# Kernel tuning notes

Hardware: AMD Instinct MI355X
Metric: run time of the kernel (lower is better)

Reference implementation:

```python
import jax, jax.numpy as jnp
import numpy as np

N_CAND = 21  # tf.linspace(0, 1, 21) candidate pool
SOFTMIN_TEMP = 100.0


def _tree_constants(max_depth: int):
    """Signed split->descendant matrix M (S,N) and node->parent one-hot P (N,N)."""
    n_splits = 2 ** max_depth - 1
    n_nodes = 2 ** (max_depth + 1) - 1
    M = np.zeros((n_splits, n_nodes), np.float32)
    for s in range(n_splits):
        for n in range(n_nodes):
            a = n
            while a > 0:
                p = (a - 1) // 2
                if p == s:
                    # left-subtree descendants get -1, right-subtree +1
                    M[s, n] = -1.0 if a == 2 * s + 1 else 1.0
                    break
                a = p
    P = np.zeros((n_nodes, n_nodes), np.float32)
    for i in range(1, n_nodes):
        P[i, (i - 1) // 2] = 1.0
    return jnp.asarray(M), jnp.asarray(P), n_splits, n_nodes


def setup_inputs() -> dict:
    key = jax.random.key(0)
    kx, kw, kb = jax.random.split(key, 3)
    B, F = 512, 512
    max_depth = 8
    n_splits = 2 ** max_depth - 1
    x = jax.random.normal(kx, (B, F), dtype=jnp.float32)
    # VarianceScaling(scale=2.0, mode='fan_in') ~ std sqrt(2/F)
    W = jax.random.normal(kw, (F, n_splits), dtype=jnp.float32) * np.sqrt(2.0 / F).astype(np.float32)
    # keras RandomNormal default stddev=0.05
    b = jax.random.normal(kb, (n_splits,), dtype=jnp.float32) * 0.05
    return {"x": x, "W": W, "b": b, "max_depth": max_depth}


def reference(x, W, b, max_depth):
    M, P, n_splits, n_nodes = _tree_constants(int(max_depth))
    # q per split, then min over ancestor splits (method 0)
    q_split = x @ W + b                                   # (B, S)
    q_bsn = q_split[:, :, None] * M[None] + 1.0 - jnp.abs(M)[None]  # (B, S, N)
    q_node = jnp.min(q_bsn, axis=1)                       # (B, N)

    a_cand = jnp.linspace(0.0, 1.0, N_CAND)               # (C,)
    qn = q_node[:, :, None]                               # (B, N, 1)
    sqr = jnp.where(a_cand <= qn + 0.5, (a_cand - (qn + 0.5)) ** 2, 0.0)
    # reg part sums over the size-1 leading axis of a -> just a^2 (reg_lambda=1.0 in call)
    g_a = 0.5 * a_cand ** 2 + 0.5 * jnp.sum(sqr, axis=0)  # (N, C)

    eye = jnp.eye(n_nodes, dtype=jnp.float32)

    def body(carry, _):
        n2g, _ = carry
        g_grp = n2g.T @ g_a                               # (N, C): group-summed objective
        w = jax.nn.softmax(-SOFTMIN_TEMP * g_grp, axis=1)
        a_grp = jnp.sum(a_cand * w, axis=1)               # (N,) soft argmin over candidates
        a_node = n2g @ a_grp                              # (N,) broadcast group value to nodes
        a_par = (P @ a_node)[1:]
        a_par = jnp.concatenate([jnp.ones((1,), a_node.dtype), a_par])
        viol = a_node - a_par
        t = jnp.argmax(viol)
        cond = (jnp.max(viol) <= 1e-8) & (t > 0)
        t_oh = jax.nn.one_hot(t, n_nodes, dtype=jnp.float32)
        p_oh = t_oh @ P
        n2g = n2g + jnp.where(cond, 1.0, 0.0) * jnp.outer(t_oh, p_oh - t_oh)
        return (n2g, a_node), None

    (_, a_node), _ = jax.lax.scan(body, (eye, jnp.zeros(n_nodes, jnp.float32)), None,
                                  length=n_nodes + 1)
    trajectory = jnp.clip(q_node, 0.0, a_node[None, :])   # (B, N)
    return trajectory
```

## Files before the change

kernel.cpp:

```cpp
#include <hip/hip_runtime.h>
#include <hip/hip_bf16.h>
#include <math.h>

#define BATCH 512
#define FDIM  512
#define NSPL  255
#define NNOD  511
#define NC    21


__global__ __launch_bounds__(256) void k_qgemm(const float* __restrict__ x,
                                               const float* __restrict__ W,
                                               float* __restrict__ partial,
                                               int fpc) {
  __shared__ float Ws[64 * 68];
  __shared__ float xT[64 * 68];
  const int tid = threadIdx.x;
  const int s0 = blockIdx.x * 64;
  const int b0 = blockIdx.y * 64;
  const int f0 = blockIdx.z * fpc;
  const int sx = tid & 15;
  const int by = tid >> 4;
  float acc[4][4];
#pragma unroll
  for (int i = 0; i < 4; ++i)
#pragma unroll
    for (int j = 0; j < 4; ++j) acc[i][j] = 0.f;

  for (int fc = f0; fc < f0 + fpc; fc += 64) {
    {
      int si = tid & 63, fr = tid >> 6;
#pragma unroll
      for (int r = 0; r < 16; ++r) {
        int fi = fr + r * 4;
        int s = s0 + si;
        Ws[fi * 68 + si] = (s < NSPL) ? W[(fc + fi) * NSPL + s] : 0.f;
      }
      int j = tid & 63, ir = tid >> 6;
#pragma unroll
      for (int r = 0; r < 16; ++r) {
        int i = ir + r * 4;
        xT[j * 68 + i] = x[(b0 + i) * FDIM + (fc + j)];
      }
    }
    __syncthreads();
#pragma unroll 8
    for (int f = 0; f < 64; ++f) {
      float4 av = *(const float4*)&Ws[f * 68 + sx * 4];
      float4 xv = *(const float4*)&xT[f * 68 + by * 4];
      const float a4[4] = {av.x, av.y, av.z, av.w};
      const float x4[4] = {xv.x, xv.y, xv.z, xv.w};
#pragma unroll
      for (int i = 0; i < 4; ++i)
#pragma unroll
        for (int j = 0; j < 4; ++j) acc[i][j] += a4[i] * x4[j];
    }
    __syncthreads();
  }

  float* pout = partial + (size_t)blockIdx.z * (256 * BATCH);
#pragma unroll
  for (int i = 0; i < 4; ++i) {
    int s = s0 + sx * 4 + i;
    if (s < NSPL) {
      float4 v = make_float4(acc[i][0], acc[i][1], acc[i][2], acc[i][3]);
      *(float4*)&pout[s * BATCH + b0 + by * 4] = v;
    }
  }
}

__global__ __launch_bounds__(256) void k_qreduce(const float* __restrict__ partial,
                                                 const float* __restrict__ bias,
                                                 float* __restrict__ qsT, int n) {
  int idx = blockIdx.x * 256 + threadIdx.x;
  if (idx >= NSPL * BATCH) return;
  int s = idx >> 9;
  float v = 0.f;
  for (int c = 0; c < n; ++c) v += partial[(size_t)c * (256 * BATCH) + idx];
  qsT[idx] = v + bias[s];
}

__global__ __launch_bounds__(256) void k_qsplitT_fb(const float* __restrict__ x,
                                                    const float* __restrict__ W,
                                                    const float* __restrict__ bias,
                                                    float* __restrict__ qsT) {
  const int s = threadIdx.x;
  const int b0 = blockIdx.x * 8;
  if (s >= NSPL) return;
  float acc0[8], acc1[8];
#pragma unroll
  for (int i = 0; i < 8; ++i) { acc0[i] = 0.f; acc1[i] = 0.f; }
#pragma unroll 2
  for (int f = 0; f < 256; ++f) {
    float w0 = W[f * NSPL + s];
    float w1 = W[(f + 256) * NSPL + s];
#pragma unroll
    for (int i = 0; i < 8; ++i) {
      acc0[i] += x[(b0 + i) * FDIM + f] * w0;
      acc1[i] += x[(b0 + i) * FDIM + f + 256] * w1;
    }
  }
  float bs = bias[s];
#pragma unroll
  for (int i = 0; i < 8; ++i) qsT[s * BATCH + b0 + i] = (acc0[i] + acc1[i]) + bs;
}

__device__ __forceinline__ float qnode_walk(const float* __restrict__ qsT, int n, int b) {
  float q = 1.0f;
  int a = n;
  while (a > 0) {
    int p = (a - 1) >> 1;
    float v = qsT[p * BATCH + b];
    q = fminf(q, (a & 1) ? -v : v);
    a = p;
  }
  return q;
}

__global__ __launch_bounds__(256) void k_ga(const float* __restrict__ qsT,
                                            float* __restrict__ ga,
                                            double* __restrict__ agrp0,
                                            float* __restrict__ qnodeT) {
  const int n = blockIdx.x;
  const int tid = threadIdx.x;
  __shared__ float qs[BATCH];
  __shared__ double part[4][NC];
  __shared__ float gaRow[NC];
  __shared__ double zS[NC];
  __shared__ double eS[NC];
  __shared__ double mS;
#pragma unroll
  for (int rep = 0; rep < 2; ++rep) {
    int b = tid + rep * 256;
    float q = qnode_walk(qsT, n, b);
    qs[b] = q;
    qnodeT[n * BATCH + b] = q;
  }
  __syncthreads();
  if (tid < 4 * NC) {
    int c = tid % NC, chunk = tid / NC;
    double ac = 0.05 * (double)c;
    double ssum = 0.0;
    int b0 = chunk * 128;
    for (int b = b0; b < b0 + 128; ++b) {
      float qh = qs[b] + 0.5f;
      double dqh = (double)qh;
      if (ac <= dqh) { double d = ac - dqh; ssum += d * d; }
    }
    part[chunk][c] = ssum;
  }
  __syncthreads();
  if (tid < NC) {
    double ac = 0.05 * (double)tid;
    double ssum = ((part[0][tid] + part[1][tid]) + part[2][tid]) + part[3][tid];
    float gv = (float)(0.5 * ac * ac + 0.5 * ssum);
    ga[n * NC + tid] = gv;
    gaRow[tid] = gv;
  }
  __syncthreads();

  if (tid < NC) zS[tid] = -100.0 * (double)gaRow[tid];
  __syncthreads();
  if (tid == 0) {
    double m = -1e300;
#pragma unroll
    for (int c = 0; c < NC; ++c) m = fmax(m, zS[c]);
    mS = m;
  }
  __syncthreads();
  if (tid < NC) eS[tid] = exp(zS[tid] - mS);
  __syncthreads();
  if (tid == 0) {
    double S = 0.0;
#pragma unroll
    for (int c = 0; c < NC; ++c) S += eS[c];
    double A = 0.0;
#pragma unroll
    for (int c = 0; c < NC; ++c) A += (0.05 * (double)c) * (eS[c] / S);
    agrp0[n] = A;
  }
}

__global__ __launch_bounds__(64) void k_scan(const float* __restrict__ ga_g,
                                             const double* __restrict__ agrp0,
                                             double* __restrict__ a_node_out) {
  __shared__ float gaS[NNOD * NC];
  __shared__ double agrp[512];
  __shared__ double anode[512];
  __shared__ float kfS[512];
  const int lane = threadIdx.x;

  {
    const float4* src = (const float4*)ga_g;
    float4* dst = (float4*)gaS;
    const int n4 = (NNOD * NC) / 4;
#pragma unroll 4
    for (int i = lane; i < n4; i += 64) dst[i] = src[i];
    if (lane < (NNOD * NC) - n4 * 4) gaS[n4 * 4 + lane] = ga_g[n4 * 4 + lane];
  }
  for (int i = lane; i < 512; i += 64) {
    agrp[i] = (i < NNOD) ? agrp0[i] : 0.0;
    anode[i] = 0.0;
    kfS[i] = 0.0f;
  }
  __syncthreads();

  int t = 0, p = 0;
  double areg[8];
  int iter = 0;
  for (;;) {
    if (iter > 0) {
      int j = lane >> 5, c = lane & 31;
      int g = j ? p : t;
      double z = -1e300;
      if (c < NC) {
        double acc = (1.0 - (double)kfS[g]) * (double)gaS[g * NC + c];
        int l = 2 * g + 1, r = 2 * g + 2;
        if (l < NNOD) acc = acc + (double)kfS[l] * (double)gaS[l * NC + c];
        if (r < NNOD) acc = acc + (double)kfS[r] * (double)gaS[r * NC + c];
        z = -100.0 * acc;
      }
      double m = z;
#pragma unroll
      for (int off = 16; off >= 1; off >>= 1) m = fmax(m, __shfl_xor(m, off, 32));
      double e = (c < NC) ? exp(z - m) : 0.0;
      double S = e;
#pragma unroll
      for (int off = 16; off >= 1; off >>= 1) S += __shfl_xor(S, off, 32);
      double term = (c < NC) ? (0.05 * (double)c) * (e / S) : 0.0;
#pragma unroll
      for (int off = 16; off >= 1; off >>= 1) term += __shfl_xor(term, off, 32);
      if (c == 0) agrp[g] = term;
      __syncthreads();
    }

#pragma unroll
    for (int u = 0; u < 8; ++u) {
      int n = lane + (u << 6);
      if (n < NNOD) {
        double kn = (double)kfS[n];
        double agn = agrp[n];
        double an;
        if (n == 0) an = agn;
        else an = kn * agrp[(n - 1) >> 1] + (1.0 - kn) * agn;
        areg[u] = an;
        anode[n] = an;
      }
    }
    __syncthreads();

    double bv = -1e300; int bi = 0x7fffffff;
#pragma unroll
    for (int u = 0; u < 8; ++u) {
      int n = lane + (u << 6);
      if (n < NNOD) {
        double ap = (n == 0) ? 1.0 : anode[(n - 1) >> 1];
        double vi = areg[u] - ap;
        if (vi > bv) { bv = vi; bi = n; }
      }
    }
#pragma unroll
    for (int off = 32; off >= 1; off >>= 1) {
      double ov = __shfl_xor(bv, off, 64);
      int oi = __shfl_xor(bi, off, 64);
      if (ov > bv || (ov == bv && oi < bi)) { bv = ov; bi = oi; }
    }

    bool cond = (bv <= 1e-8) && (bi > 0);
    if (!cond || iter == 511) break;
    t = bi; p = (t - 1) >> 1;
    if (lane == 0) kfS[t] += 1.0f;
    __syncthreads();
    ++iter;
  }

#pragma unroll
  for (int u = 0; u < 8; ++u) {
    int n = lane + (u << 6);
    if (n < NNOD) a_node_out[n] = areg[u];
  }
}

__global__ __launch_bounds__(256) void k_clip(const float* __restrict__ qnodeT,
                                              const double* __restrict__ a_node,
                                              float* __restrict__ out) {
  __shared__ float tile[64][65];
  __shared__ double anS[64];
  const int n0 = blockIdx.x * 64;
  const int b0 = blockIdx.y * 64;
  const int tid = threadIdx.x;
  if (tid < 64) anS[tid] = (n0 + tid < NNOD) ? a_node[n0 + tid] : 0.0;
  for (int i = tid; i < 64 * 64; i += 256) {
    int ni = i >> 6, bj = i & 63;
    int nn = n0 + ni;
    tile[ni][bj] = (nn < NNOD) ? qnodeT[nn * BATCH + b0 + bj] : 0.f;
  }
  __syncthreads();
  for (int i = tid; i < 64 * 64; i += 256) {
    int bi = i >> 6, nj = i & 63;
    int nn = n0 + nj;
    if (nn < NNOD) {
      float q = tile[nj][bi];
      double r = fmin(fmax((double)q, 0.0), anS[nj]);
      out[(size_t)(b0 + bi) * NNOD + nn] = (float)r;
    }
  }
}

extern "C" void kernel_launch(void* const* d_in, const int* in_sizes, int n_in,
                              void* d_out, int out_size, void* d_ws, size_t ws_size,
                              hipStream_t stream) {
  (void)in_sizes; (void)n_in; (void)out_size;
  const float* x    = (const float*)d_in[0];
  const float* W    = (const float*)d_in[1];
  const float* bias = (const float*)d_in[2];
  float* out = (float*)d_out;

  char* ws = (char*)d_ws;
  const size_t PART_STRIDE = 256 * BATCH * sizeof(float);
  const size_t QS = 524288;
  const size_t QN = 1048576;
  const size_t GA = 43008;
  const size_t AG = 4096;
  const size_t AN = 4096;
  const size_t TAIL = QS + QN + GA + AG + AN;

  int n = 8;
  while (n > 1 && (size_t)n * PART_STRIDE + TAIL > ws_size) n >>= 1;
  bool splitk_ok = ((size_t)n * PART_STRIDE + TAIL <= ws_size);

  size_t P = splitk_ok ? (size_t)n * PART_STRIDE : 0;
  float*  qsT    = (float*) (ws + P);
  float*  qnodeT = (float*) (ws + P + QS);
  float*  ga     = (float*) (ws + P + QS + QN);
  double* agrp0  = (double*)(ws + P + QS + QN + GA);
  double* a_node = (double*)(ws + P + QS + QN + GA + AG);

  if (splitk_ok) {
    float* partial = (float*)ws;
    k_qgemm<<<dim3(4, 8, n), dim3(256), 0, stream>>>(x, W, partial, 512 / n);
    k_qreduce<<<dim3(510), dim3(256), 0, stream>>>(partial, bias, qsT, n);
  } else {
    k_qsplitT_fb<<<dim3(64), dim3(256), 0, stream>>>(x, W, bias, qsT);
  }
  k_ga<<<dim3(NNOD), dim3(256), 0, stream>>>(qsT, ga, agrp0, qnodeT);
  k_scan<<<dim3(1), dim3(64), 0, stream>>>(ga, agrp0, a_node);
  k_clip<<<dim3(8, 8), dim3(256), 0, stream>>>(qnodeT, a_node, out);
}
```

Measured before the change: 96.31 us.

## Replace split-K GEMM plus reduce with single-pass GEMM writing qsT directly

The split-K GEMM, which wrote partial sums to workspace, and its separate reduction kernel are replaced by one kernel. That kernel covers the full feature dimension per block, with a 16-split by 64-batch tile, and adds the bias before writing qsT. This removes one kernel launch and the round trip of the partial buffers through global memory. In exchange, each thread does far less register reuse (1x4 per thread instead of 4x4), so each output costs more shared-memory loads. The grid becomes 128 blocks with no split-K parallelism, and the GEMM runs serially over K.

```diff
diff --git a/kernel.cpp b/kernel.cpp
--- a/kernel.cpp
+++ b/kernel.cpp
@@ -9,32 +9,32 @@
 #define NC    21
 
 
-__global__ __launch_bounds__(256) void k_qgemm(const float* __restrict__ x,
-                                               const float* __restrict__ W,
-                                               float* __restrict__ partial,
-                                               int fpc) {
-  __shared__ float Ws[64 * 68];
+__global__ __launch_bounds__(256) void k_qgemm2(const float* __restrict__ x,
+                                                const float* __restrict__ W,
+                                                const float* __restrict__ bias,
+                                                float* __restrict__ qsT) {
+  __shared__ float Ws[64 * 17];
   __shared__ float xT[64 * 68];
   const int tid = threadIdx.x;
-  const int s0 = blockIdx.x * 64;
+  const int s0 = blockIdx.x * 16;
   const int b0 = blockIdx.y * 64;
-  const int f0 = blockIdx.z * fpc;
-  const int sx = tid & 15;
-  const int by = tid >> 4;
-  float acc[4][4];
-#pragma unroll
-  for (int i = 0; i < 4; ++i)
-#pragma unroll
-    for (int j = 0; j < 4; ++j) acc[i][j] = 0.f;
-
-  for (int fc = f0; fc < f0 + fpc; fc += 64) {
+  const int sl = tid >> 4;
+  const int bq = tid & 15;
+  const int s = s0 + sl;
+
+  float acc[4];
+  float vsum[4];
+#pragma unroll
+  for (int j = 0; j < 4; ++j) { acc[j] = 0.f; vsum[j] = 0.f; }
+
+  for (int fc = 0; fc < FDIM; fc += 64) {
     {
-      int si = tid & 63, fr = tid >> 6;
-#pragma unroll
-      for (int r = 0; r < 16; ++r) {
-        int fi = fr + r * 4;
-        int s = s0 + si;
-        Ws[fi * 68 + si] = (s < NSPL) ? W[(fc + fi) * NSPL + s] : 0.f;
+      int si = tid & 15, f4 = tid >> 4;
+#pragma unroll
+      for (int r = 0; r < 4; ++r) {
+        int fi = f4 + r * 16;
+        int ss = s0 + si;
+        Ws[fi * 17 + si] = (ss < NSPL) ? W[(fc + fi) * NSPL + ss] : 0.f;
       }
       int j = tid & 63, ir = tid >> 6;
 #pragma unroll
@@ -46,38 +46,23 @@
     __syncthreads();
 #pragma unroll 8
     for (int f = 0; f < 64; ++f) {
-      float4 av = *(const float4*)&Ws[f * 68 + sx * 4];
-      float4 xv = *(const float4*)&xT[f * 68 + by * 4];
-      const float a4[4] = {av.x, av.y, av.z, av.w};
+      float w = Ws[f * 17 + sl];
+      float4 xv = *(const float4*)&xT[f * 68 + bq * 4];
       const float x4[4] = {xv.x, xv.y, xv.z, xv.w};
 #pragma unroll
-      for (int i = 0; i < 4; ++i)
-#pragma unroll
-        for (int j = 0; j < 4; ++j) acc[i][j] += a4[i] * x4[j];
-    }
+      for (int j = 0; j < 4; ++j) acc[j] += w * x4[j];
+    }
+#pragma unroll
+    for (int j = 0; j < 4; ++j) { vsum[j] += acc[j]; acc[j] = 0.f; }
     __syncthreads();
   }
 
-  float* pout = partial + (size_t)blockIdx.z * (256 * BATCH);
-#pragma unroll
-  for (int i = 0; i < 4; ++i) {
-    int s = s0 + sx * 4 + i;
-    if (s < NSPL) {
-      float4 v = make_float4(acc[i][0], acc[i][1], acc[i][2], acc[i][3]);
-      *(float4*)&pout[s * BATCH + b0 + by * 4] = v;
-    }
-  }
-}
-
-__global__ __launch_bounds__(256) void k_qreduce(const float* __restrict__ partial,
-                                                 const float* __restrict__ bias,
-                                                 float* __restrict__ qsT, int n) {
-  int idx = blockIdx.x * 256 + threadIdx.x;
-  if (idx >= NSPL * BATCH) return;
-  int s = idx >> 9;
-  float v = 0.f;
-  for (int c = 0; c < n; ++c) v += partial[(size_t)c * (256 * BATCH) + idx];
-  qsT[idx] = v + bias[s];
+  if (s < NSPL) {
+    float bs = bias[s];
+#pragma unroll
+    for (int j = 0; j < 4; ++j)
+      qsT[s * BATCH + b0 + bq * 4 + j] = vsum[j] + bs;
+  }
 }
 
 __global__ __launch_bounds__(256) void k_qsplitT_fb(const float* __restrict__ x,
@@ -317,32 +302,18 @@
   float* out = (float*)d_out;
 
   char* ws = (char*)d_ws;
-  const size_t PART_STRIDE = 256 * BATCH * sizeof(float);
   const size_t QS = 524288;
   const size_t QN = 1048576;
   const size_t GA = 43008;
   const size_t AG = 4096;
-  const size_t AN = 4096;
-  const size_t TAIL = QS + QN + GA + AG + AN;
-
-  int n = 8;
-  while (n > 1 && (size_t)n * PART_STRIDE + TAIL > ws_size) n >>= 1;
-  bool splitk_ok = ((size_t)n * PART_STRIDE + TAIL <= ws_size);
-
-  size_t P = splitk_ok ? (size_t)n * PART_STRIDE : 0;
-  float*  qsT    = (float*) (ws + P);
-  float*  qnodeT = (float*) (ws + P + QS);
-  float*  ga     = (float*) (ws + P + QS + QN);
-  double* agrp0  = (double*)(ws + P + QS + QN + GA);
-  double* a_node = (double*)(ws + P + QS + QN + GA + AG);
-
-  if (splitk_ok) {
-    float* partial = (float*)ws;
-    k_qgemm<<<dim3(4, 8, n), dim3(256), 0, stream>>>(x, W, partial, 512 / n);
-    k_qreduce<<<dim3(510), dim3(256), 0, stream>>>(partial, bias, qsT, n);
-  } else {
-    k_qsplitT_fb<<<dim3(64), dim3(256), 0, stream>>>(x, W, bias, qsT);
-  }
+
+  float*  qsT    = (float*) (ws);
+  float*  qnodeT = (float*) (ws + QS);
+  float*  ga     = (float*) (ws + QS + QN);
+  double* agrp0  = (double*)(ws + QS + QN + GA);
+  double* a_node = (double*)(ws + QS + QN + GA + AG);
+
+  k_qgemm2<<<dim3(16, 8), dim3(256), 0, stream>>>(x, W, bias, qsT);
   k_ga<<<dim3(NNOD), dim3(256), 0, stream>>>(qsT, ga, agrp0, qnodeT);
   k_scan<<<dim3(1), dim3(64), 0, stream>>>(ga, agrp0, a_node);
   k_clip<<<dim3(8, 8), dim3(256), 0, stream>>>(qnodeT, a_node, out);
```

After: 113.1 us. 17.4% more time.

## Fuse GEMM, reduce and g_a stages into one cooperative kernel with grid syncs

Applied to the files above, without the earlier changes.

Merges the split-K GEMM, partial reduction and per-node g_a kernels into a single cooperative launch of 511 blocks, using grid.sync between stages instead of separate kernel launches. This removes two kernel launch boundaries and their gaps. The cost is grid-wide barrier overhead and a combined shared-memory footprint that may lower occupancy. A fallback to the original three-kernel path is kept for when cooperative launch is unavailable.

```diff
diff --git a/kernel.cpp b/kernel.cpp
--- a/kernel.cpp
+++ b/kernel.cpp
@@ -1,6 +1,9 @@
 #include <hip/hip_runtime.h>
+#include <hip/hip_cooperative_groups.h>
 #include <hip/hip_bf16.h>
 #include <math.h>
+
+namespace cg = cooperative_groups;
 
 #define BATCH 512
 #define FDIM  512
@@ -9,16 +12,15 @@
 #define NC    21
 
 
-__global__ __launch_bounds__(256) void k_qgemm(const float* __restrict__ x,
-                                               const float* __restrict__ W,
-                                               float* __restrict__ partial,
-                                               int fpc) {
+__device__ __forceinline__ void gemm_body(const float* __restrict__ x,
+                                          const float* __restrict__ W,
+                                          float* __restrict__ partial,
+                                          int fpc, int bx, int byy, int bz, int tid) {
   __shared__ float Ws[64 * 68];
   __shared__ float xT[64 * 68];
-  const int tid = threadIdx.x;
-  const int s0 = blockIdx.x * 64;
-  const int b0 = blockIdx.y * 64;
-  const int f0 = blockIdx.z * fpc;
+  const int s0 = bx * 64;
+  const int b0 = byy * 64;
+  const int f0 = bz * fpc;
   const int sx = tid & 15;
   const int by = tid >> 4;
   float acc[4][4];
@@ -58,7 +60,7 @@
     __syncthreads();
   }
 
-  float* pout = partial + (size_t)blockIdx.z * (256 * BATCH);
+  float* pout = partial + (size_t)bz * (256 * BATCH);
 #pragma unroll
   for (int i = 0; i < 4; ++i) {
     int s = s0 + sx * 4 + i;
@@ -69,40 +71,17 @@
   }
 }
 
-__global__ __launch_bounds__(256) void k_qreduce(const float* __restrict__ partial,
-                                                 const float* __restrict__ bias,
-                                                 float* __restrict__ qsT, int n) {
-  int idx = blockIdx.x * 256 + threadIdx.x;
-  if (idx >= NSPL * BATCH) return;
-  int s = idx >> 9;
-  float v = 0.f;
-  for (int c = 0; c < n; ++c) v += partial[(size_t)c * (256 * BATCH) + idx];
-  qsT[idx] = v + bias[s];
-}
-
-__global__ __launch_bounds__(256) void k_qsplitT_fb(const float* __restrict__ x,
-                                                    const float* __restrict__ W,
-                                                    const float* __restrict__ bias,
-                                                    float* __restrict__ qsT) {
-  const int s = threadIdx.x;
-  const int b0 = blockIdx.x * 8;
-  if (s >= NSPL) return;
-  float acc0[8], acc1[8];
-#pragma unroll
-  for (int i = 0; i < 8; ++i) { acc0[i] = 0.f; acc1[i] = 0.f; }
-#pragma unroll 2
-  for (int f = 0; f < 256; ++f) {
-    float w0 = W[f * NSPL + s];
-    float w1 = W[(f + 256) * NSPL + s];
-#pragma unroll
-    for (int i = 0; i < 8; ++i) {
-      acc0[i] += x[(b0 + i) * FDIM + f] * w0;
-      acc1[i] += x[(b0 + i) * FDIM + f + 256] * w1;
-    }
-  }
-  float bs = bias[s];
-#pragma unroll
-  for (int i = 0; i < 8; ++i) qsT[s * BATCH + b0 + i] = (acc0[i] + acc1[i]) + bs;
+__device__ __forceinline__ void reduce_body(const float* __restrict__ partial,
+                                            const float* __restrict__ bias,
+                                            float* __restrict__ qsT, int n,
+                                            int bid, int tid) {
+  int idx = bid * 256 + tid;
+  if (idx < NSPL * BATCH) {
+    int s = idx >> 9;
+    float v = 0.f;
+    for (int c = 0; c < n; ++c) v += partial[(size_t)c * (256 * BATCH) + idx];
+    qsT[idx] = v + bias[s];
+  }
 }
 
 __device__ __forceinline__ float qnode_walk(const float* __restrict__ qsT, int n, int b) {
@@ -117,12 +96,11 @@
   return q;
 }
 
-__global__ __launch_bounds__(256) void k_ga(const float* __restrict__ qsT,
-                                            float* __restrict__ ga,
-                                            double* __restrict__ agrp0,
-                                            float* __restrict__ qnodeT) {
-  const int n = blockIdx.x;
-  const int tid = threadIdx.x;
+__device__ __forceinline__ void ga_body(const float* __restrict__ qsT,
+                                        float* __restrict__ ga,
+                                        double* __restrict__ agrp0,
+                                        float* __restrict__ qnodeT,
+                                        int n, int tid) {
   __shared__ float qs[BATCH];
   __shared__ double part[4][NC];
   __shared__ float gaRow[NC];
@@ -179,6 +157,72 @@
     for (int c = 0; c < NC; ++c) A += (0.05 * (double)c) * (eS[c] / S);
     agrp0[n] = A;
   }
+}
+
+__global__ __launch_bounds__(256) void k_qgemm(const float* __restrict__ x,
+                                               const float* __restrict__ W,
+                                               float* __restrict__ partial,
+                                               int fpc) {
+  gemm_body(x, W, partial, fpc, blockIdx.x, blockIdx.y, blockIdx.z, threadIdx.x);
+}
+
+__global__ __launch_bounds__(256) void k_qreduce(const float* __restrict__ partial,
+                                                 const float* __restrict__ bias,
+                                                 float* __restrict__ qsT, int n) {
+  reduce_body(partial, bias, qsT, n, blockIdx.x, threadIdx.x);
+}
+
+__global__ __launch_bounds__(256) void k_ga(const float* __restrict__ qsT,
+                                            float* __restrict__ ga,
+                                            double* __restrict__ agrp0,
+                                            float* __restrict__ qnodeT) {
+  ga_body(qsT, ga, agrp0, qnodeT, blockIdx.x, threadIdx.x);
+}
+
+__global__ __launch_bounds__(256) void k_qsplitT_fb(const float* __restrict__ x,
+                                                    const float* __restrict__ W,
+                                                    const float* __restrict__ bias,
+                                                    float* __restrict__ qsT) {
+  const int s = threadIdx.x;
+  const int b0 = blockIdx.x * 8;
+  if (s >= NSPL) return;
+  float acc0[8], acc1[8];
+#pragma unroll
+  for (int i = 0; i < 8; ++i) { acc0[i] = 0.f; acc1[i] = 0.f; }
+#pragma unroll 2
+  for (int f = 0; f < 256; ++f) {
+    float w0 = W[f * NSPL + s];
+    float w1 = W[(f + 256) * NSPL + s];
+#pragma unroll
+    for (int i = 0; i < 8; ++i) {
+      acc0[i] += x[(b0 + i) * FDIM + f] * w0;
+      acc1[i] += x[(b0 + i) * FDIM + f + 256] * w1;
+    }
+  }
+  float bs = bias[s];
+#pragma unroll
+  for (int i = 0; i < 8; ++i) qsT[s * BATCH + b0 + i] = (acc0[i] + acc1[i]) + bs;
+}
+
+__global__ __launch_bounds__(256) void k_front(const float* __restrict__ x,
+                                               const float* __restrict__ W,
+                                               const float* __restrict__ bias,
+                                               float* __restrict__ partial,
+                                               float* __restrict__ qsT,
+                                               float* __restrict__ ga,
+                                               double* __restrict__ agrp0,
+                                               float* __restrict__ qnodeT) {
+  const int tid = threadIdx.x;
+  const int bid = blockIdx.x;
+  cg::grid_group grid = cg::this_grid();
+
+  if (bid < 256)
+    gemm_body(x, W, partial, 64, bid & 3, (bid >> 2) & 7, bid >> 5, tid);
+  grid.sync();
+  if (bid < 510)
+    reduce_body(partial, bias, qsT, 8, bid, tid);
+  grid.sync();
+  ga_body(qsT, ga, agrp0, qnodeT, bid, tid);
 }
 
 __global__ __launch_bounds__(64) void k_scan(const float* __restrict__ ga_g,
@@ -336,14 +380,37 @@
   double* agrp0  = (double*)(ws + P + QS + QN + GA);
   double* a_node = (double*)(ws + P + QS + QN + GA + AG);
 
-  if (splitk_ok) {
+  static int coop_state = -1;
+  if (coop_state < 0) {
+    int dev = 0, cu = 0, nb = 0;
+    hipError_t e0 = hipGetDevice(&dev);
+    hipError_t e1 = hipDeviceGetAttribute(&cu, hipDeviceAttributeMultiprocessorCount, dev);
+    hipError_t e2 = hipOccupancyMaxActiveBlocksPerMultiprocessor(&nb, k_front, 256, 0);
+    coop_state = (e0 == hipSuccess && e1 == hipSuccess && e2 == hipSuccess &&
+                  (long)nb * (long)cu >= NNOD) ? 1 : 0;
+  }
+
+  bool front_done = false;
+  if (splitk_ok && n == 8 && coop_state == 1) {
     float* partial = (float*)ws;
-    k_qgemm<<<dim3(4, 8, n), dim3(256), 0, stream>>>(x, W, partial, 512 / n);
-    k_qreduce<<<dim3(510), dim3(256), 0, stream>>>(partial, bias, qsT, n);
-  } else {
-    k_qsplitT_fb<<<dim3(64), dim3(256), 0, stream>>>(x, W, bias, qsT);
-  }
-  k_ga<<<dim3(NNOD), dim3(256), 0, stream>>>(qsT, ga, agrp0, qnodeT);
+    void* args[] = {(void*)&x, (void*)&W, (void*)&bias, (void*)&partial,
+                    (void*)&qsT, (void*)&ga, (void*)&agrp0, (void*)&qnodeT};
+    hipError_t e = hipLaunchCooperativeKernel((const void*)k_front, dim3(NNOD),
+                                              dim3(256), args, 0, stream);
+    if (e == hipSuccess) front_done = true;
+    else coop_state = 0;
+  }
+
+  if (!front_done) {
+    if (splitk_ok) {
+      float* partial = (float*)ws;
+      k_qgemm<<<dim3(4, 8, n), dim3(256), 0, stream>>>(x, W, partial, 512 / n);
+      k_qreduce<<<dim3(510), dim3(256), 0, stream>>>(partial, bias, qsT, n);
+    } else {
+      k_qsplitT_fb<<<dim3(64), dim3(256), 0, stream>>>(x, W, bias, qsT);
+    }
+    k_ga<<<dim3(NNOD), dim3(256), 0, stream>>>(qsT, ga, agrp0, qnodeT);
+  }
   k_scan<<<dim3(1), dim3(64), 0, stream>>>(ga, agrp0, a_node);
   k_clip<<<dim3(8, 8), dim3(256), 0, stream>>>(qnodeT, a_node, out);
 }
```

Result: slower. 223.8 us (+132.4%).
